# Optimization experiments

Measured on AMD Instinct MI355X. Metric: run time of the kernel, lower is better.

Reference implementation:

```python
import jax, jax.numpy as jnp
import numpy as np

WIDTH = 64
HEIGHT = 64
FEAT = 128
LAT = 64
NUM_SLOTS = 7


def pixel_coords(img_size):
    g = jnp.linspace(-1.0, 1.0, img_size)
    g1, g2 = jnp.meshgrid(g, g, indexing='ij')  # matches torch.meshgrid default
    return jnp.stack([g1, g2], axis=0)[None]  # (1, 2, S, S)


def clamp_pg(x, lo, hi):
    # clamp that preserves gradients (straight-through)
    return x + jax.lax.stop_gradient(jnp.clip(x, lo, hi) - x)


def setup_inputs() -> dict:
    key = jax.random.key(0)
    k0, k1, k2, k3 = jax.random.split(key, 4)
    bs = 64
    x = jax.random.normal(k0, (bs, FEAT, WIDTH, HEIGHT), jnp.float32)
    rand_pixel = jax.random.uniform(k1, (bs, 1, WIDTH, HEIGHT), jnp.float32)
    conv_w = jax.random.normal(k2, (LAT, FEAT), jnp.float32) / np.sqrt(FEAT)
    conv_b = jax.random.normal(k3, (LAT,), jnp.float32) * 0.01
    gate = jnp.asarray(0.5, jnp.float32)  # ScalarGate parameter (nonzero so c_f is non-degenerate)
    # laplacian kernel: sigma_init = 1 / (sqrt(num_slots) * log 2)
    log_sigma = jnp.asarray(np.log(1.0 / (np.sqrt(NUM_SLOTS) * np.log(2.0))), jnp.float32)
    return {'x': x, 'rand_pixel': rand_pixel, 'conv_w': conv_w, 'conv_b': conv_b,
            'gate': gate, 'log_sigma': log_sigma, 'num_cl_steps': 6}


def _forward(x, rand_pixel, conv_w, conv_b, gate, log_sigma, num_cl_steps):
    bs = x.shape[0]
    # SemiConv: gated 1x1 conv + fixed uv coordinate channels
    out = gate * (jnp.einsum('of,bfhw->bohw', conv_w, x) + conv_b[None, :, None, None])
    uv = jnp.concatenate([jnp.zeros((1, LAT - 2, WIDTH, HEIGHT), out.dtype),
                          pixel_coords(WIDTH).astype(out.dtype)], axis=1)
    c_f = out + uv                      # (bs, LAT, W, H)
    delta = out[:, -2:]                 # (bs, 2, W, H)
    sigma = jnp.exp(log_sigma)
    c_flat = c_f.reshape(bs, LAT, -1)   # (bs, LAT, W*H)
    b_idx = jnp.arange(bs)
    log_s0 = jnp.zeros((bs, 1, WIDTH, HEIGHT), c_f.dtype)

    def step(log_s, _):
        # interpolate-to-same-size is identity -> scope = exp(log_s)
        probs = (rand_pixel * jnp.exp(log_s)).reshape(bs, -1)
        idx = jnp.argmax(probs, axis=1)                 # (bs,)
        seed = c_flat[b_idx, :, idx]                    # (bs, LAT)
        diff = c_f - seed[:, :, None, None]
        dist = jnp.sqrt(clamp_pg((diff ** 2).sum(1), 1e-10, 1e10))  # euclidian (laplacian kernel)
        alpha = jnp.exp(-dist / sigma)[:, None]         # (bs, 1, W, H)
        alpha = clamp_pg(alpha, 0.01, 0.99)
        log_m = log_s + jnp.log(alpha)
        new_log_s = log_s + jnp.log1p(-alpha)
        return new_log_s, (log_m, new_log_s, seed)

    log_s_final, (log_m_steps, log_s_steps, seeds) = jax.lax.scan(
        step, log_s0, None, length=num_cl_steps)
    # log_m_k has num_cl_steps masks plus the final scope appended
    log_m_k = jnp.concatenate([log_m_steps, log_s_final[None]], axis=0)
    log_s_k = jnp.concatenate([log_s0[None], log_s_steps], axis=0)
    return log_m_k, log_s_k, c_f, delta, seeds


def reference(x, rand_pixel, conv_w, conv_b, gate, log_sigma, num_cl_steps):
    return _forward(x, rand_pixel, conv_w, conv_b, gate, log_sigma, num_cl_steps)
```

## Files before the change

kernel.cpp:

```cpp
#include <hip/hip_runtime.h>
#include <hip/hip_bf16.h>

#define NPIX 4096
#define FEAT 128
#define LAT 64
#define BS 64
#define NSTEPS 6

#define OFF_LOGM  0u
#define OFF_LOGS  1835008u
#define OFF_CF    3670016u
#define OFF_DELTA 20447232u
#define OFF_SEEDS 20971520u

typedef float f32x4 __attribute__((ext_vector_type(4)));
typedef short s16x8 __attribute__((ext_vector_type(8)));

__device__ __forceinline__ void amax_comb(float& bv, int& bi, float v, int i) {
    if (v > bv || (v == bv && i < bi)) { bv = v; bi = i; }
}

__device__ __forceinline__ short f2bf_rne(float r) {
    __hip_bfloat16 h = __float2bfloat16(r);
    return __builtin_bit_cast(short, h);
}

__device__ __forceinline__ void split2(float v, short& hi, short& lo) {
    unsigned u = __builtin_bit_cast(unsigned, v);
    hi = (short)(u >> 16);
    float hf = __builtin_bit_cast(float, u & 0xFFFF0000u);
    lo = f2bf_rne(v - hf);
}

__global__ __launch_bounds__(256, 2) void conv_mfma(
    const float* __restrict__ x, const float* __restrict__ rand_pixel,
    const float* __restrict__ w, const float* __restrict__ bias,
    const float* __restrict__ gate_p, float* __restrict__ out,
    float* __restrict__ pval, int* __restrict__ pidx, int* __restrict__ cnt)
{
    __shared__ __align__(16) short Whi[64][136];
    __shared__ __align__(16) short Wlo[64][136];
    __shared__ float sbias[64];

    const int tid  = threadIdx.x;
    const int b    = blockIdx.x >> 4;
    const int tile = blockIdx.x & 15;
    const int p0   = tile * 256;
    const int lane = tid & 63;
    const int wv   = tid >> 6;
    const int l15  = lane & 15;
    const int lg   = lane >> 4;

    const float gate = gate_p[0];

    if (tile == 0 && wv == 0 && lane < 8) cnt[b * 8 + lane] = 0;

    #pragma unroll
    for (int i = 0; i < 8; ++i) {
        int q = i * 256 + tid;
        int o = q >> 5;
        int f = (q & 31) * 4;
        float4 wq = *(const float4*)(w + o * 128 + f);
        short h0, l0, h1, l1, h2, l2, h3, l3;
        split2(gate * wq.x, h0, l0);
        split2(gate * wq.y, h1, l1);
        split2(gate * wq.z, h2, l2);
        split2(gate * wq.w, h3, l3);
        *(short4*)&Whi[o][f] = make_short4(h0, h1, h2, h3);
        *(short4*)&Wlo[o][f] = make_short4(l0, l1, l2, l3);
    }
    if (tid < 64) sbias[tid] = gate * bias[tid];
    __syncthreads();

    f32x4 acc[4][4];
    #pragma unroll
    for (int og = 0; og < 4; ++og)
        #pragma unroll
        for (int pg = 0; pg < 4; ++pg)
            acc[og][pg] = (f32x4){0.f, 0.f, 0.f, 0.f};

    const float* xb = x + (size_t)b * FEAT * NPIX + p0 + wv * 64;

    #pragma unroll
    for (int kc = 0; kc < 4; ++kc) {
        s16x8 Ah[4], Al[4];
        #pragma unroll
        for (int og = 0; og < 4; ++og) {
            Ah[og] = *(const s16x8*)&Whi[og * 16 + l15][kc * 32 + lg * 8];
            Al[og] = *(const s16x8*)&Wlo[og * 16 + l15][kc * 32 + lg * 8];
        }
        #pragma unroll
        for (int pg = 0; pg < 4; ++pg) {
            const float* xp = xb + pg * 16 + l15;
            const int fb = kc * 32 + lg * 8;
            float xv[8];
            #pragma unroll
            for (int e = 0; e < 8; ++e)
                xv[e] = xp[(size_t)(fb + e) * NPIX];
            s16x8 Bh, Bl;
            #pragma unroll
            for (int e = 0; e < 8; ++e) {
                short h, l;
                split2(xv[e], h, l);
                Bh[e] = h; Bl[e] = l;
            }
            #pragma unroll
            for (int og = 0; og < 4; ++og) {
                acc[og][pg] = __builtin_amdgcn_mfma_f32_16x16x32_bf16(Ah[og], Bh, acc[og][pg], 0, 0, 0);
                acc[og][pg] = __builtin_amdgcn_mfma_f32_16x16x32_bf16(Ah[og], Bl, acc[og][pg], 0, 0, 0);
                acc[og][pg] = __builtin_amdgcn_mfma_f32_16x16x32_bf16(Al[og], Bh, acc[og][pg], 0, 0, 0);
            }
        }
    }

    float* cf = out + OFF_CF + (size_t)b * LAT * NPIX;
    #pragma unroll
    for (int og = 0; og < 4; ++og) {
        #pragma unroll
        for (int pg = 0; pg < 4; ++pg) {
            #pragma unroll
            for (int r = 0; r < 4; ++r) {
                int o = og * 16 + lg * 4 + r;
                int p = p0 + wv * 64 + pg * 16 + l15;
                float v = acc[og][pg][r] + sbias[o];
                if (o == 62) {
                    out[OFF_DELTA + ((size_t)b * 2 + 0) * NPIX + p] = v;
                    v += (float)(-1.0 + 2.0 * (double)(p >> 6) / 63.0);
                } else if (o == 63) {
                    out[OFF_DELTA + ((size_t)b * 2 + 1) * NPIX + p] = v;
                    v += (float)(-1.0 + 2.0 * (double)(p & 63) / 63.0);
                }
                cf[(size_t)o * NPIX + p] = v;
            }
        }
    }

    if (wv == 0) {
        *(float4*)(out + OFF_LOGS + (size_t)b * NPIX + p0 + lane * 4) =
            make_float4(0.f, 0.f, 0.f, 0.f);
        float4 rv = *(const float4*)(rand_pixel + (size_t)b * NPIX + p0 + lane * 4);
        int pb = p0 + lane * 4;
        float bv = rv.x; int bi = pb;
        if (rv.y > bv) { bv = rv.y; bi = pb + 1; }
        if (rv.z > bv) { bv = rv.z; bi = pb + 2; }
        if (rv.w > bv) { bv = rv.w; bi = pb + 3; }
        #pragma unroll
        for (int off = 32; off > 0; off >>= 1) {
            float ov = __shfl_down(bv, off, 64);
            int   oi = __shfl_down(bi, off, 64);
            amax_comb(bv, bi, ov, oi);
        }
        if (lane == 0) { pval[blockIdx.x] = bv; pidx[blockIdx.x] = bi; }
    }
}

#define REP16(OP) OP(0) OP(1) OP(2) OP(3) OP(4) OP(5) OP(6) OP(7) \
                  OP(8) OP(9) OP(10) OP(11) OP(12) OP(13) OP(14) OP(15)

__global__ __launch_bounds__(1024) void steps_fused(
    const float* __restrict__ rand_pixel, const float* __restrict__ log_sigma_p,
    float* __restrict__ out, float* pv, int* pi, int* cnt)
{
    __shared__ float s_mv[16];
    __shared__ int   s_mi[16];
    __shared__ __align__(16) float s_seed[LAT];
    __shared__ float s_rv[16];
    __shared__ int   s_ri[16];

    const int tid  = threadIdx.x;
    const int b    = blockIdx.x >> 2;
    const int tile = blockIdx.x & 3;
    const int p    = tile * 1024 + tid;

    const float* cfb = out + OFF_CF + (size_t)b * LAT * NPIX;

#define DECLR(i) f32x4 r##i;
    REP16(DECLR)
#define LOADR(i) r##i = (f32x4){ cfb[(size_t)(4*i+0)*NPIX + p], cfb[(size_t)(4*i+1)*NPIX + p], \
                                 cfb[(size_t)(4*i+2)*NPIX + p], cfb[(size_t)(4*i+3)*NPIX + p] };
    REP16(LOADR)

    f32x4 aq = r0 * r0;
#define SQR(i) aq += r##i * r##i;
    SQR(1) SQR(2) SQR(3) SQR(4) SQR(5) SQR(6) SQR(7)
    SQR(8) SQR(9) SQR(10) SQR(11) SQR(12) SQR(13) SQR(14) SQR(15)
    const float cr2 = aq[0] + aq[1] + aq[2] + aq[3];

    const float rp    = rand_pixel[(size_t)b * NPIX + p];
    const float sigma = expf(log_sigma_p[0]);
    float ls = 0.f;

    #pragma unroll 1
    for (int s = 0; s < NSTEPS; ++s) {
        if (s > 0) {
            if (tid == 0) {
                while (__hip_atomic_load(&cnt[b * 8 + s], __ATOMIC_ACQUIRE,
                                         __HIP_MEMORY_SCOPE_AGENT) < 4)
                    __builtin_amdgcn_s_sleep(2);
            }
            __syncthreads();
        }
        const int nmerge = (s == 0) ? 16 : 4;
        if (tid < nmerge) {
            s_mv[tid] = __hip_atomic_load(&pv[(s * BS + b) * 16 + tid],
                                          __ATOMIC_RELAXED, __HIP_MEMORY_SCOPE_AGENT);
            s_mi[tid] = __hip_atomic_load(&pi[(s * BS + b) * 16 + tid],
                                          __ATOMIC_RELAXED, __HIP_MEMORY_SCOPE_AGENT);
        }
        __syncthreads();

        float bv = -1.0f; int bi = 0;
        for (int k = 0; k < nmerge; ++k) amax_comb(bv, bi, s_mv[k], s_mi[k]);

        if (tid < LAT) s_seed[tid] = cfb[(size_t)tid * NPIX + bi];
        __syncthreads();
        if (tile == 0 && tid < LAT)
            out[OFF_SEEDS + ((size_t)s * BS + b) * LAT + tid] = s_seed[tid];

        f32x4 dacc = (f32x4){0.f, 0.f, 0.f, 0.f};
        f32x4 sacc = (f32x4){0.f, 0.f, 0.f, 0.f};
#define DOT(i) { f32x4 sv = *(const f32x4*)&s_seed[4*i]; dacc += r##i * sv; sacc += sv * sv; }
        REP16(DOT)
        float dot = dacc[0] + dacc[1] + dacc[2] + dacc[3];
        float s2  = sacc[0] + sacc[1] + sacc[2] + sacc[3];
        float d2  = cr2 + s2 - 2.0f * dot;

        float dist  = sqrtf(fminf(fmaxf(d2, 1e-10f), 1e10f));
        float alpha = expf(-dist / sigma);
        alpha = fminf(fmaxf(alpha, 0.01f), 0.99f);
        float lm  = ls + logf(alpha);
        float lsn = ls + log1pf(-alpha);

        out[OFF_LOGM + ((size_t)s * BS + b) * NPIX + p]       = lm;
        out[OFF_LOGS + ((size_t)(s + 1) * BS + b) * NPIX + p] = lsn;
        ls = lsn;

        if (s == NSTEPS - 1) {
            out[OFF_LOGM + ((size_t)NSTEPS * BS + b) * NPIX + p] = lsn;
        } else {
            float prob = rp * expf(lsn);
            int   idx  = p;
            #pragma unroll
            for (int off = 32; off > 0; off >>= 1) {
                float ov = __shfl_down(prob, off, 64);
                int   oi = __shfl_down(idx, off, 64);
                amax_comb(prob, idx, ov, oi);
            }
            int lane = tid & 63, wid = tid >> 6;
            if (lane == 0) { s_rv[wid] = prob; s_ri[wid] = idx; }
            __syncthreads();
            if (tid == 0) {
                float fb = s_rv[0]; int fi = s_ri[0];
                #pragma unroll
                for (int k = 1; k < 16; ++k) amax_comb(fb, fi, s_rv[k], s_ri[k]);
                __hip_atomic_store(&pv[((s + 1) * BS + b) * 16 + tile], fb,
                                   __ATOMIC_RELAXED, __HIP_MEMORY_SCOPE_AGENT);
                __hip_atomic_store(&pi[((s + 1) * BS + b) * 16 + tile], fi,
                                   __ATOMIC_RELAXED, __HIP_MEMORY_SCOPE_AGENT);
                __hip_atomic_fetch_add(&cnt[b * 8 + s + 1], 1,
                                       __ATOMIC_RELEASE, __HIP_MEMORY_SCOPE_AGENT);
            }
        }
    }
}

__global__ __launch_bounds__(1024) void step_kernel(
    const float* __restrict__ rand_pixel, const float* __restrict__ log_sigma_p,
    float* __restrict__ out, float* pv, int* pi, int step)
{
    __shared__ float s_mv[16];
    __shared__ int   s_mi[16];
    __shared__ __align__(16) float s_seed[LAT];
    __shared__ float s_rv[16];
    __shared__ int   s_ri[16];

    const int tid  = threadIdx.x;
    const int b    = blockIdx.x >> 2;
    const int tile = blockIdx.x & 3;
    const int p    = tile * 1024 + tid;

    const float* cfb = out + OFF_CF + (size_t)b * LAT * NPIX;

    const int nmerge = (step == 0) ? 16 : 4;
    if (tid < nmerge) { s_mv[tid] = pv[(step * BS + b) * 16 + tid];
                        s_mi[tid] = pi[(step * BS + b) * 16 + tid]; }
    __syncthreads();
    float bv = -1.0f; int bi = 0;
    for (int k = 0; k < nmerge; ++k) amax_comb(bv, bi, s_mv[k], s_mi[k]);

    if (tid < LAT) s_seed[tid] = cfb[(size_t)tid * NPIX + bi];
    __syncthreads();
    if (tile == 0 && tid < LAT)
        out[OFF_SEEDS + ((size_t)step * BS + b) * LAT + tid] = s_seed[tid];

    float d2 = 0.f;
    #pragma unroll
    for (int c = 0; c < LAT; ++c) {
        float d = cfb[(size_t)c * NPIX + p] - s_seed[c];
        d2 = fmaf(d, d, d2);
    }
    float dist  = sqrtf(fminf(fmaxf(d2, 1e-10f), 1e10f));
    float sigma = expf(log_sigma_p[0]);
    float alpha = expf(-dist / sigma);
    alpha = fminf(fmaxf(alpha, 0.01f), 0.99f);

    float ls  = out[OFF_LOGS + ((size_t)step * BS + b) * NPIX + p];
    float lm  = ls + logf(alpha);
    float lsn = ls + log1pf(-alpha);

    out[OFF_LOGM + ((size_t)step * BS + b) * NPIX + p]       = lm;
    out[OFF_LOGS + ((size_t)(step + 1) * BS + b) * NPIX + p] = lsn;
    if (step == NSTEPS - 1)
        out[OFF_LOGM + ((size_t)NSTEPS * BS + b) * NPIX + p] = lsn;

    if (step < NSTEPS - 1) {
        float prob = rand_pixel[(size_t)b * NPIX + p] * expf(lsn);
        int   idx  = p;
        #pragma unroll
        for (int off = 32; off > 0; off >>= 1) {
            float ov = __shfl_down(prob, off, 64);
            int   oi = __shfl_down(idx, off, 64);
            amax_comb(prob, idx, ov, oi);
        }
        int lane = tid & 63, wid = tid >> 6;
        if (lane == 0) { s_rv[wid] = prob; s_ri[wid] = idx; }
        __syncthreads();
        if (tid == 0) {
            float fb = s_rv[0]; int fi = s_ri[0];
            #pragma unroll
            for (int k = 1; k < 16; ++k) amax_comb(fb, fi, s_rv[k], s_ri[k]);
            pv[((step + 1) * BS + b) * 16 + tile] = fb;
            pi[((step + 1) * BS + b) * 16 + tile] = fi;
        }
    }
}

extern "C" void kernel_launch(void* const* d_in, const int* in_sizes, int n_in,
                              void* d_out, int out_size, void* d_ws, size_t ws_size,
                              hipStream_t stream) {
    const float* x          = (const float*)d_in[0];
    const float* rand_pixel = (const float*)d_in[1];
    const float* w          = (const float*)d_in[2];
    const float* bias       = (const float*)d_in[3];
    const float* gate       = (const float*)d_in[4];
    const float* log_sigma  = (const float*)d_in[5];

    float* out = (float*)d_out;
    float* pv  = (float*)d_ws;
    int*   pi  = (int*)((char*)d_ws + 24576);
    int*   cnt = (int*)((char*)d_ws + 49152);

    conv_mfma<<<1024, 256, 0, stream>>>(x, rand_pixel, w, bias, gate, out, pv, pi, cnt);

    const float* a0 = rand_pixel; const float* a1 = log_sigma; float* a2 = out;
    float* a3 = pv; int* a4 = pi; int* a5 = cnt;
    void* kp[6] = {(void*)&a0, (void*)&a1, (void*)&a2, (void*)&a3, (void*)&a4, (void*)&a5};
    hipError_t e = hipLaunchCooperativeKernel((const void*)steps_fused,
                                              dim3(256), dim3(1024), kp, 0, stream);
    if (e != hipSuccess) {
        for (int s = 0; s < NSTEPS; ++s)
            step_kernel<<<256, 1024, 0, stream>>>(rand_pixel, log_sigma, out, pv, pi, s);
    }
}
```

Baseline: 134.3 us.

## Stage x via vectorized loads and LDS transpose, precompute split weights in separate kernel

Conv input is now loaded as float4 per thread, transposed across 4 lanes with shuffles, split into bf16 hi/lo once and staged in shared memory, instead of each lane doing scalar strided loads and redundant splits per MFMA tile. Weights are optionally pre-split by a small prep kernel into workspace and read directly from global, which frees LDS and allows higher occupancy (launch bound 4). The steps kernel also loads c_f with float4 plus shuffle transpose. This adds two syncthreads per k-chunk, an extra kernel launch, and depends on workspace size for the fast path.

```diff
diff --git a/kernel.cpp b/kernel.cpp
--- a/kernel.cpp
+++ b/kernel.cpp
@@ -15,6 +15,7 @@
 
 typedef float f32x4 __attribute__((ext_vector_type(4)));
 typedef short s16x8 __attribute__((ext_vector_type(8)));
+typedef short s16x4 __attribute__((ext_vector_type(4)));
 
 __device__ __forceinline__ void amax_comb(float& bv, int& bi, float v, int i) {
     if (v > bv || (v == bv && i < bi)) { bv = v; bi = i; }
@@ -32,14 +33,41 @@
     lo = f2bf_rne(v - hf);
 }
 
-__global__ __launch_bounds__(256, 2) void conv_mfma(
+__device__ __forceinline__ void transpose4(float4& v, int b) {
+    float4 w;
+    w.x = __shfl_xor(v.x, 1, 64); w.y = __shfl_xor(v.y, 1, 64);
+    w.z = __shfl_xor(v.z, 1, 64); w.w = __shfl_xor(v.w, 1, 64);
+    float4 u;
+    if ((b & 1) == 0) u = make_float4(v.x, w.x, v.z, w.z);
+    else              u = make_float4(w.y, v.y, w.w, v.w);
+    float4 w2;
+    w2.x = __shfl_xor(u.x, 2, 64); w2.y = __shfl_xor(u.y, 2, 64);
+    w2.z = __shfl_xor(u.z, 2, 64); w2.w = __shfl_xor(u.w, 2, 64);
+    if ((b & 2) == 0) v = make_float4(u.x, u.y, w2.x, w2.y);
+    else              v = make_float4(w2.z, w2.w, u.z, u.w);
+}
+
+__global__ void prep_w(const float* __restrict__ w, const float* __restrict__ gate_p,
+                       short* __restrict__ gwh, short* __restrict__ gwl)
+{
+    int i = blockIdx.x * 256 + threadIdx.x;
+    float v = gate_p[0] * w[i];
+    short h, l; split2(v, h, l);
+    gwh[i] = h; gwl[i] = l;
+}
+
+template<bool PRE>
+__global__ __launch_bounds__(256, PRE ? 4 : 2) void conv_mfma(
     const float* __restrict__ x, const float* __restrict__ rand_pixel,
     const float* __restrict__ w, const float* __restrict__ bias,
     const float* __restrict__ gate_p, float* __restrict__ out,
-    float* __restrict__ pval, int* __restrict__ pidx, int* __restrict__ cnt)
+    float* __restrict__ pval, int* __restrict__ pidx, int* __restrict__ cnt,
+    const short* __restrict__ gwh, const short* __restrict__ gwl)
 {
-    __shared__ __align__(16) short Whi[64][136];
-    __shared__ __align__(16) short Wlo[64][136];
+    __shared__ __align__(16) short Xhi[256][36];
+    __shared__ __align__(16) short Xlo[256][36];
+    __shared__ __align__(16) short Whi[PRE ? 1 : 64][PRE ? 1 : 136];
+    __shared__ __align__(16) short Wlo[PRE ? 1 : 64][PRE ? 1 : 136];
     __shared__ float sbias[64];
 
     const int tid  = threadIdx.x;
@@ -51,26 +79,26 @@
     const int l15  = lane & 15;
     const int lg   = lane >> 4;
 
-    const float gate = gate_p[0];
-
     if (tile == 0 && wv == 0 && lane < 8) cnt[b * 8 + lane] = 0;
 
-    #pragma unroll
-    for (int i = 0; i < 8; ++i) {
-        int q = i * 256 + tid;
-        int o = q >> 5;
-        int f = (q & 31) * 4;
-        float4 wq = *(const float4*)(w + o * 128 + f);
-        short h0, l0, h1, l1, h2, l2, h3, l3;
-        split2(gate * wq.x, h0, l0);
-        split2(gate * wq.y, h1, l1);
-        split2(gate * wq.z, h2, l2);
-        split2(gate * wq.w, h3, l3);
-        *(short4*)&Whi[o][f] = make_short4(h0, h1, h2, h3);
-        *(short4*)&Wlo[o][f] = make_short4(l0, l1, l2, l3);
-    }
-    if (tid < 64) sbias[tid] = gate * bias[tid];
-    __syncthreads();
+    if constexpr (!PRE) {
+        const float gate = gate_p[0];
+        #pragma unroll
+        for (int i = 0; i < 8; ++i) {
+            int q = i * 256 + tid;
+            int o = q >> 5;
+            int f = (q & 31) * 4;
+            float4 wq = *(const float4*)(w + o * 128 + f);
+            short h0, l0, h1, l1, h2, l2, h3, l3;
+            split2(gate * wq.x, h0, l0);
+            split2(gate * wq.y, h1, l1);
+            split2(gate * wq.z, h2, l2);
+            split2(gate * wq.w, h3, l3);
+            *(short4*)&Whi[o][f] = make_short4(h0, h1, h2, h3);
+            *(short4*)&Wlo[o][f] = make_short4(l0, l1, l2, l3);
+        }
+    }
+    if (tid < 64) sbias[tid] = gate_p[0] * bias[tid];
 
     f32x4 acc[4][4];
     #pragma unroll
@@ -79,31 +107,46 @@
         for (int pg = 0; pg < 4; ++pg)
             acc[og][pg] = (f32x4){0.f, 0.f, 0.f, 0.f};
 
-    const float* xb = x + (size_t)b * FEAT * NPIX + p0 + wv * 64;
-
-    #pragma unroll
+    const float* xb = x + (size_t)b * FEAT * NPIX + p0;
+
     for (int kc = 0; kc < 4; ++kc) {
+        __syncthreads();
+        const float* xc = xb + (size_t)(kc * 32) * NPIX + (tid & ~3);
+        #pragma unroll
+        for (int i = 0; i < 8; ++i) {
+            float4 v = *(const float4*)(xc + (size_t)(i * 4 + (tid & 3)) * NPIX);
+            transpose4(v, tid & 3);
+            short h0, l0, h1, l1, h2, l2, h3, l3;
+            split2(v.x, h0, l0);
+            split2(v.y, h1, l1);
+            split2(v.z, h2, l2);
+            split2(v.w, h3, l3);
+            *(short4*)&Xhi[tid][i * 4] = make_short4(h0, h1, h2, h3);
+            *(short4*)&Xlo[tid][i * 4] = make_short4(l0, l1, l2, l3);
+        }
+        __syncthreads();
+
         s16x8 Ah[4], Al[4];
         #pragma unroll
         for (int og = 0; og < 4; ++og) {
-            Ah[og] = *(const s16x8*)&Whi[og * 16 + l15][kc * 32 + lg * 8];
-            Al[og] = *(const s16x8*)&Wlo[og * 16 + l15][kc * 32 + lg * 8];
-        }
+            if constexpr (PRE) {
+                Ah[og] = *(const s16x8*)&gwh[(og * 16 + l15) * 128 + kc * 32 + lg * 8];
+                Al[og] = *(const s16x8*)&gwl[(og * 16 + l15) * 128 + kc * 32 + lg * 8];
+            } else {
+                Ah[og] = *(const s16x8*)&Whi[og * 16 + l15][kc * 32 + lg * 8];
+                Al[og] = *(const s16x8*)&Wlo[og * 16 + l15][kc * 32 + lg * 8];
+            }
+        }
+
         #pragma unroll
         for (int pg = 0; pg < 4; ++pg) {
-            const float* xp = xb + pg * 16 + l15;
-            const int fb = kc * 32 + lg * 8;
-            float xv[8];
-            #pragma unroll
-            for (int e = 0; e < 8; ++e)
-                xv[e] = xp[(size_t)(fb + e) * NPIX];
-            s16x8 Bh, Bl;
-            #pragma unroll
-            for (int e = 0; e < 8; ++e) {
-                short h, l;
-                split2(xv[e], h, l);
-                Bh[e] = h; Bl[e] = l;
-            }
+            int pxl = wv * 64 + pg * 16 + l15;
+            const short* ph = &Xhi[pxl][lg * 8];
+            const short* pl = &Xlo[pxl][lg * 8];
+            s16x4 h0 = *(const s16x4*)ph, h1 = *(const s16x4*)(ph + 4);
+            s16x4 q0 = *(const s16x4*)pl, q1 = *(const s16x4*)(pl + 4);
+            s16x8 Bh = {h0[0], h0[1], h0[2], h0[3], h1[0], h1[1], h1[2], h1[3]};
+            s16x8 Bl = {q0[0], q0[1], q0[2], q0[3], q1[0], q1[1], q1[2], q1[3]};
             #pragma unroll
             for (int og = 0; og < 4; ++og) {
                 acc[og][pg] = __builtin_amdgcn_mfma_f32_16x16x32_bf16(Ah[og], Bh, acc[og][pg], 0, 0, 0);
@@ -176,8 +219,10 @@
 
 #define DECLR(i) f32x4 r##i;
     REP16(DECLR)
-#define LOADR(i) r##i = (f32x4){ cfb[(size_t)(4*i+0)*NPIX + p], cfb[(size_t)(4*i+1)*NPIX + p], \
-                                 cfb[(size_t)(4*i+2)*NPIX + p], cfb[(size_t)(4*i+3)*NPIX + p] };
+#define LOADR(i) { \
+        float4 v = *(const float4*)(cfb + (size_t)(4*i + (tid & 3)) * NPIX + tile * 1024 + (tid & ~3)); \
+        transpose4(v, tid & 3); \
+        r##i = (f32x4){v.x, v.y, v.z, v.w}; }
     REP16(LOADR)
 
     f32x4 aq = r0 * r0;
@@ -349,8 +394,19 @@
     float* pv  = (float*)d_ws;
     int*   pi  = (int*)((char*)d_ws + 24576);
     int*   cnt = (int*)((char*)d_ws + 49152);
-
-    conv_mfma<<<1024, 256, 0, stream>>>(x, rand_pixel, w, bias, gate, out, pv, pi, cnt);
+    short* gwh = (short*)((char*)d_ws + 51200);
+    short* gwl = (short*)((char*)d_ws + 67584);
+
+    const bool pre = (ws_size >= 100 * 1024);
+
+    if (pre) {
+        prep_w<<<32, 256, 0, stream>>>(w, gate, gwh, gwl);
+        conv_mfma<true><<<1024, 256, 0, stream>>>(x, rand_pixel, w, bias, gate, out,
+                                                  pv, pi, cnt, gwh, gwl);
+    } else {
+        conv_mfma<false><<<1024, 256, 0, stream>>>(x, rand_pixel, w, bias, gate, out,
+                                                   pv, pi, cnt, nullptr, nullptr);
+    }
 
     const float* a0 = rand_pixel; const float* a1 = log_sigma; float* a2 = out;
     float* a3 = pv; int* a4 = pi; int* a5 = cnt;
```

New measurement: 145.6 us. 1.08x slower.
